# Kernel tuning notes

Hardware: AMD Instinct MI355X
Metric: run time of the kernel (lower is better)

Reference implementation:

```python
import jax, jax.numpy as jnp
import numpy as np

N_NODES = 10000
N_EDGES = 160000
D = 512
DROPOUT_P = 0.5
NEG_SLOPE = 0.25


def setup_inputs() -> dict:
    key = jax.random.key(0)
    ks = jax.random.split(key, 8)
    H = jax.random.normal(ks[0], (N_NODES, D), dtype=jnp.float32)
    rows = jax.random.randint(ks[1], (N_EDGES,), 0, N_NODES)
    cols = jax.random.randint(ks[2], (N_EDGES,), 0, N_NODES)
    vals = jax.random.uniform(ks[3], (N_EDGES,), dtype=jnp.float32)
    # xavier-normal-ish weights, zero bias (matches torch init)
    std = float(np.sqrt(2.0 / (D + D)))
    W1 = jax.random.normal(ks[4], (D, D), dtype=jnp.float32) * std
    b1 = jnp.zeros((D,), dtype=jnp.float32)
    W2 = jax.random.normal(ks[5], (D, D), dtype=jnp.float32) * std
    b2 = jnp.zeros((D,), dtype=jnp.float32)
    return {"H": H, "rows": rows, "cols": cols, "vals": vals,
            "W1": W1, "b1": b1, "W2": W2, "b2": b2}


def _spmm(rows, cols, vals, dense):
    # sparse [N,N] @ dense [N,D] via gather + segment-sum
    gathered = vals[:, None] * dense[cols]          # [E, D]
    return jax.ops.segment_sum(gathered, rows, num_segments=N_NODES)


def _leaky_relu(x):
    return jnp.where(x >= 0, x, NEG_SLOPE * x)


def reference(H, rows, cols, vals, W1, b1, W2, b2):
    # layer 1: dense GEMM -> SpMM -> bias -> leaky_relu -> dropout(training=True)
    h = _spmm(rows, cols, vals, H @ W1) + b1
    h = _leaky_relu(h)
    keep = jax.random.bernoulli(jax.random.key(42), 1.0 - DROPOUT_P, h.shape)
    h = jnp.where(keep, h / (1.0 - DROPOUT_P), 0.0)
    # layer 2
    h = _spmm(rows, cols, vals, h @ W2) + b2
    return _leaky_relu(h)
```

## Files before the change

kernel.cpp:

```cpp
#include <hip/hip_runtime.h>
#include <stdint.h>

#define N_NODES 10000
#define M_PAD   10112
#define N_EDGES 160000
#define DIM     512
#define N_ELEMS 5120000
#define NEG_SLOPE 0.25f

typedef short     short8 __attribute__((ext_vector_type(8)));
typedef __bf16    bf16x8 __attribute__((ext_vector_type(8)));
typedef float     f32x4  __attribute__((ext_vector_type(4)));

__device__ __forceinline__ unsigned short f2bf(float f) {
    uint32_t u = __builtin_bit_cast(uint32_t, f);
    uint32_t r = (u + 0x7fffu + ((u >> 16) & 1u)) >> 16;
    return (unsigned short)r;
}
__device__ __forceinline__ float b2f(unsigned short u) {
    return __builtin_bit_cast(float, (uint32_t)u << 16);
}

__device__ __forceinline__ uint32_t rotl32(uint32_t x, uint32_t d) {
    return (x << d) | (x >> (32u - d));
}
__device__ __forceinline__ void threefry_42(uint32_t x0, uint32_t x1,
                                            uint32_t& o0, uint32_t& o1) {
    const uint32_t ks0 = 0u, ks1 = 42u, ks2 = 0x1BD11BDAu ^ 42u;
    x0 += ks0; x1 += ks1;
#define TF_R4(a,b,c,d) \
    x0 += x1; x1 = rotl32(x1,a); x1 ^= x0; \
    x0 += x1; x1 = rotl32(x1,b); x1 ^= x0; \
    x0 += x1; x1 = rotl32(x1,c); x1 ^= x0; \
    x0 += x1; x1 = rotl32(x1,d); x1 ^= x0;
    TF_R4(13,15,26,6);  x0 += ks1; x1 += ks2 + 1u;
    TF_R4(17,29,16,24); x0 += ks2; x1 += ks0 + 2u;
    TF_R4(13,15,26,6);  x0 += ks0; x1 += ks1 + 3u;
    TF_R4(17,29,16,24); x0 += ks1; x1 += ks2 + 4u;
    TF_R4(13,15,26,6);  x0 += ks2; x1 += ks0 + 5u;
#undef TF_R4
    o0 = x0; o1 = x1;
}

__global__ void hist_kernel(const int* __restrict__ rows, int* __restrict__ cnt) {
    int e = blockIdx.x * blockDim.x + threadIdx.x;
    if (e < N_EDGES) atomicAdd(&cnt[rows[e]], 1);
}

__global__ __launch_bounds__(1024)
void scan_kernel(const int* __restrict__ cnt, int* __restrict__ rs, int* __restrict__ cur) {
    __shared__ int s[1024];
    int t = threadIdx.x;
    int base_i = t * 10;
    int local[10];
    int p = 0;
    if (t < 1000) {
        #pragma unroll
        for (int j = 0; j < 10; ++j) { local[j] = cnt[base_i + j]; p += local[j]; }
    }
    s[t] = p;
    __syncthreads();
    for (int off = 1; off < 1024; off <<= 1) {
        int v = (t >= off) ? s[t - off] : 0;
        __syncthreads();
        s[t] += v;
        __syncthreads();
    }
    if (t < 1000) {
        int run = s[t] - p;
        #pragma unroll
        for (int j = 0; j < 10; ++j) {
            rs[base_i + j]  = run;
            cur[base_i + j] = run;
            run += local[j];
        }
        if (t == 999) rs[N_NODES] = run;
    }
}

__global__ void scatter_kernel(const int* __restrict__ rows, const int* __restrict__ cols,
                               const float* __restrict__ vals, int* __restrict__ cur,
                               int* __restrict__ scol, float* __restrict__ sval) {
    int e = blockIdx.x * blockDim.x + threadIdx.x;
    if (e < N_EDGES) {
        int r = rows[e];
        int p = atomicAdd(&cur[r], 1);
        scol[p] = cols[e];
        sval[p] = vals[e];
    }
}

__global__ void convert_kernel(const float* __restrict__ src, unsigned short* __restrict__ dst) {
    int i = blockIdx.x * blockDim.x + threadIdx.x;
    if (i * 4 >= N_ELEMS) return;
    float4 v = ((const float4*)src)[i];
    ushort4 o;
    o.x = f2bf(v.x); o.y = f2bf(v.y); o.z = f2bf(v.z); o.w = f2bf(v.w);
    ((ushort4*)dst)[i] = o;
}

__global__ __launch_bounds__(256)
void transpose_kernel(const float* __restrict__ W, unsigned short* __restrict__ WT) {
    __shared__ float t[64][65];
    int k0 = blockIdx.x * 64, n0 = blockIdx.y * 64;
    int tx = threadIdx.x & 15, ty = threadIdx.x >> 4;
    #pragma unroll
    for (int i = 0; i < 4; ++i) {
        int k = i * 16 + ty;
        float4 v = *(const float4*)&W[(size_t)(k0 + k) * DIM + n0 + tx * 4];
        t[k][tx * 4 + 0] = v.x; t[k][tx * 4 + 1] = v.y;
        t[k][tx * 4 + 2] = v.z; t[k][tx * 4 + 3] = v.w;
    }
    __syncthreads();
    #pragma unroll
    for (int i = 0; i < 4; ++i) {
        int n = i * 16 + ty;
        ushort4 o;
        o.x = f2bf(t[tx * 4 + 0][n]); o.y = f2bf(t[tx * 4 + 1][n]);
        o.z = f2bf(t[tx * 4 + 2][n]); o.w = f2bf(t[tx * 4 + 3][n]);
        *(ushort4*)&WT[(size_t)(n0 + n) * DIM + k0 + tx * 4] = o;
    }
}

__global__ __launch_bounds__(256)
void mfma_gemm(const unsigned short* __restrict__ A, const unsigned short* __restrict__ BT,
               unsigned short* __restrict__ C, int M) {
    __shared__ short8 As[1024];
    __shared__ short8 Bs[1024];
    int tid  = threadIdx.x;
    int wid  = tid >> 6, lane = tid & 63;
    int bm   = blockIdx.x * 128;
    int bn   = blockIdx.y * 128;
    int wm   = (wid >> 1) * 64, wn = (wid & 1) * 64;

    f32x4 acc[4][4] = {};

    int srow = lane >> 3;
    int sslot = lane & 7;

    for (int k0 = 0; k0 < DIM; k0 += 64) {
        #pragma unroll
        for (int c = 0; c < 4; ++c) {
            int chunk = wid * 4 + c;
            int r  = chunk * 8 + srow;
            int ks = sslot ^ (r & 7);
            const unsigned short* ga = A  + (size_t)(bm + r) * DIM + k0 + ks * 8;
            const unsigned short* gb = BT + (size_t)(bn + r) * DIM + k0 + ks * 8;
            __builtin_amdgcn_global_load_lds(
                (const __attribute__((address_space(1))) void*)ga,
                (__attribute__((address_space(3))) void*)&As[chunk * 64], 16, 0, 0);
            __builtin_amdgcn_global_load_lds(
                (const __attribute__((address_space(1))) void*)gb,
                (__attribute__((address_space(3))) void*)&Bs[chunk * 64], 16, 0, 0);
        }
        __syncthreads();

        int lrow = lane & 15;
        int kgrp = lane >> 4;
        #pragma unroll
        for (int ks = 0; ks < 2; ++ks) {
            short8 af[4], bfr[4];
            #pragma unroll
            for (int i = 0; i < 4; ++i) {
                int r = wm + i * 16 + lrow;
                af[i]  = As[r * 8 + ((ks * 4 + kgrp) ^ (r & 7))];
                int n = wn + i * 16 + lrow;
                bfr[i] = Bs[n * 8 + ((ks * 4 + kgrp) ^ (n & 7))];
            }
            #pragma unroll
            for (int i = 0; i < 4; ++i)
                #pragma unroll
                for (int j = 0; j < 4; ++j)
                    acc[i][j] = __builtin_amdgcn_mfma_f32_16x16x32_bf16(
                        __builtin_bit_cast(bf16x8, af[i]),
                        __builtin_bit_cast(bf16x8, bfr[j]), acc[i][j], 0, 0, 0);
        }
        __syncthreads();
    }

    int crow = (lane >> 4) * 4;
    int ccol = lane & 15;
    #pragma unroll
    for (int i = 0; i < 4; ++i) {
        #pragma unroll
        for (int r = 0; r < 4; ++r) {
            int row = bm + wm + i * 16 + crow + r;
            if (row < M) {
                size_t base = (size_t)row * DIM + bn + wn + ccol;
                #pragma unroll
                for (int j = 0; j < 4; ++j)
                    C[base + j * 16] = f2bf(acc[i][j][r]);
            }
        }
    }
}

__global__ __launch_bounds__(128)
void spmm1_kernel(const unsigned short* __restrict__ X, const int* __restrict__ rs,
                  const int* __restrict__ scol, const float* __restrict__ sval,
                  const float* __restrict__ bias, unsigned short* __restrict__ hout) {
    int row = blockIdx.x;
    int t = threadIdx.x;
    int start = rs[row], end = rs[row + 1];
    const ushort4* X4 = (const ushort4*)X;
    float a0 = 0.f, a1 = 0.f, a2 = 0.f, a3 = 0.f;
    float c0 = 0.f, c1 = 0.f, c2 = 0.f, c3 = 0.f;
    int p = start;
    for (; p + 1 < end; p += 2) {
        int   i0 = scol[p], i1 = scol[p + 1];
        float v0 = sval[p], v1 = sval[p + 1];
        ushort4 x0 = X4[(size_t)i0 * 128 + t];
        ushort4 x1 = X4[(size_t)i1 * 128 + t];
        a0 = fmaf(v0, b2f(x0.x), a0); a1 = fmaf(v0, b2f(x0.y), a1);
        a2 = fmaf(v0, b2f(x0.z), a2); a3 = fmaf(v0, b2f(x0.w), a3);
        c0 = fmaf(v1, b2f(x1.x), c0); c1 = fmaf(v1, b2f(x1.y), c1);
        c2 = fmaf(v1, b2f(x1.z), c2); c3 = fmaf(v1, b2f(x1.w), c3);
    }
    if (p < end) {
        int i0 = scol[p]; float v0 = sval[p];
        ushort4 x0 = X4[(size_t)i0 * 128 + t];
        a0 = fmaf(v0, b2f(x0.x), a0); a1 = fmaf(v0, b2f(x0.y), a1);
        a2 = fmaf(v0, b2f(x0.z), a2); a3 = fmaf(v0, b2f(x0.w), a3);
    }
    float r[4];
    float4 b = *(const float4*)&bias[t * 4];
    r[0] = a0 + c0 + b.x; r[1] = a1 + c1 + b.y;
    r[2] = a2 + c2 + b.z; r[3] = a3 + c3 + b.w;
    uint32_t e0 = (uint32_t)row * DIM + t * 4;
    #pragma unroll
    for (int j = 0; j < 4; ++j) {
        float v = r[j];
        v = (v >= 0.f) ? v : NEG_SLOPE * v;
        uint32_t o0, o1;
        threefry_42(0u, e0 + j, o0, o1);
        uint32_t bits = o0 ^ o1;
        r[j] = ((int)bits >= 0) ? v * 2.0f : 0.0f;
    }
    ushort4 o;
    o.x = f2bf(r[0]); o.y = f2bf(r[1]); o.z = f2bf(r[2]); o.w = f2bf(r[3]);
    ((ushort4*)hout)[(size_t)row * 128 + t] = o;
}

__global__ __launch_bounds__(128)
void spmm2_kernel(const unsigned short* __restrict__ X, const int* __restrict__ rs,
                  const int* __restrict__ scol, const float* __restrict__ sval,
                  const float* __restrict__ bias, float* __restrict__ out) {
    int row = blockIdx.x;
    int t = threadIdx.x;
    int start = rs[row], end = rs[row + 1];
    const ushort4* X4 = (const ushort4*)X;
    float a0 = 0.f, a1 = 0.f, a2 = 0.f, a3 = 0.f;
    float c0 = 0.f, c1 = 0.f, c2 = 0.f, c3 = 0.f;
    int p = start;
    for (; p + 1 < end; p += 2) {
        int   i0 = scol[p], i1 = scol[p + 1];
        float v0 = sval[p], v1 = sval[p + 1];
        ushort4 x0 = X4[(size_t)i0 * 128 + t];
        ushort4 x1 = X4[(size_t)i1 * 128 + t];
        a0 = fmaf(v0, b2f(x0.x), a0); a1 = fmaf(v0, b2f(x0.y), a1);
        a2 = fmaf(v0, b2f(x0.z), a2); a3 = fmaf(v0, b2f(x0.w), a3);
        c0 = fmaf(v1, b2f(x1.x), c0); c1 = fmaf(v1, b2f(x1.y), c1);
        c2 = fmaf(v1, b2f(x1.z), c2); c3 = fmaf(v1, b2f(x1.w), c3);
    }
    if (p < end) {
        int i0 = scol[p]; float v0 = sval[p];
        ushort4 x0 = X4[(size_t)i0 * 128 + t];
        a0 = fmaf(v0, b2f(x0.x), a0); a1 = fmaf(v0, b2f(x0.y), a1);
        a2 = fmaf(v0, b2f(x0.z), a2); a3 = fmaf(v0, b2f(x0.w), a3);
    }
    float4 b = *(const float4*)&bias[t * 4];
    float4 r;
    r.x = a0 + c0 + b.x; r.y = a1 + c1 + b.y;
    r.z = a2 + c2 + b.z; r.w = a3 + c3 + b.w;
    r.x = (r.x >= 0.f) ? r.x : NEG_SLOPE * r.x;
    r.y = (r.y >= 0.f) ? r.y : NEG_SLOPE * r.y;
    r.z = (r.z >= 0.f) ? r.z : NEG_SLOPE * r.z;
    r.w = (r.w >= 0.f) ? r.w : NEG_SLOPE * r.w;
    ((float4*)out)[(size_t)row * 128 + t] = r;
}

extern "C" void kernel_launch(void* const* d_in, const int* in_sizes, int n_in,
                              void* d_out, int out_size, void* d_ws, size_t ws_size,
                              hipStream_t stream) {
    const float* H    = (const float*)d_in[0];
    const int*   rows = (const int*)  d_in[1];
    const int*   cols = (const int*)  d_in[2];
    const float* vals = (const float*)d_in[3];
    const float* W1   = (const float*)d_in[4];
    const float* b1   = (const float*)d_in[5];
    const float* W2   = (const float*)d_in[6];
    const float* b2   = (const float*)d_in[7];
    float* out = (float*)d_out;

    char* ws = (char*)d_ws;
    size_t off = 0;
    auto alloc = [&](size_t bytes) -> void* {
        off = (off + 255) & ~(size_t)255;
        void* p = ws + off;
        off += bytes;
        return p;
    };
    int*   cnt  = (int*)  alloc((size_t)N_NODES * 4);
    int*   rs   = (int*)  alloc((size_t)(N_NODES + 1) * 4);
    int*   cur  = (int*)  alloc((size_t)N_NODES * 4);
    int*   scol = (int*)  alloc((size_t)N_EDGES * 4);
    float* sval = (float*)alloc((size_t)N_EDGES * 4);
    unsigned short* WT1 = (unsigned short*)alloc((size_t)DIM * DIM * 2);
    unsigned short* WT2 = (unsigned short*)alloc((size_t)DIM * DIM * 2);
    unsigned short* Abf = (unsigned short*)alloc((size_t)M_PAD * DIM * 2);
    unsigned short* hbf = (unsigned short*)alloc((size_t)M_PAD * DIM * 2);
    unsigned short* Xbf = (unsigned short*)alloc((size_t)N_NODES * DIM * 2);

    convert_kernel<<<(N_ELEMS / 4 + 255) / 256, 256, 0, stream>>>(H, Abf);
    dim3 tgrid(DIM / 64, DIM / 64);
    transpose_kernel<<<tgrid, 256, 0, stream>>>(W1, WT1);
    transpose_kernel<<<tgrid, 256, 0, stream>>>(W2, WT2);
    hipMemsetAsync(cnt, 0, (size_t)N_NODES * 4, stream);
    hist_kernel<<<(N_EDGES + 255) / 256, 256, 0, stream>>>(rows, cnt);
    scan_kernel<<<1, 1024, 0, stream>>>(cnt, rs, cur);
    scatter_kernel<<<(N_EDGES + 255) / 256, 256, 0, stream>>>(rows, cols, vals, cur, scol, sval);

    dim3 ggrid(M_PAD / 128, DIM / 128);
    mfma_gemm<<<ggrid, 256, 0, stream>>>(Abf, WT1, Xbf, N_NODES);
    spmm1_kernel<<<N_NODES, 128, 0, stream>>>(Xbf, rs, scol, sval, b1, hbf);
    mfma_gemm<<<ggrid, 256, 0, stream>>>(hbf, WT2, Xbf, N_NODES);
    spmm2_kernel<<<N_NODES, 128, 0, stream>>>(Xbf, rs, scol, sval, b2, out);
}
```

Measured before the change: 126.9 us.

## Fuse prep kernels into one launch, precompute dropout bitmask, unroll SpMM by four

Merges the H-to-bf16 conversion, both weight transposes and the zeroing of the histogram counter into one multi-role prep kernel, which removes several launches and a memset. The same kernel precomputes the dropout keep mask as a packed bitmask, so spmm1 reads one word per eight threads instead of running Threefry per element. The SpMM inner loops are unrolled to four edges to keep more gathers in flight. The cost is a 640KB mask write and read, and Threefry now runs in a separate stage that can overlap the conversion work.

```diff
diff --git a/kernel.cpp b/kernel.cpp
--- a/kernel.cpp
+++ b/kernel.cpp
@@ -8,9 +8,9 @@
 #define N_ELEMS 5120000
 #define NEG_SLOPE 0.25f
 
-typedef short     short8 __attribute__((ext_vector_type(8)));
-typedef __bf16    bf16x8 __attribute__((ext_vector_type(8)));
-typedef float     f32x4  __attribute__((ext_vector_type(4)));
+typedef short          short8   __attribute__((ext_vector_type(8)));
+typedef __bf16         bf16x8   __attribute__((ext_vector_type(8)));
+typedef float          f32x4    __attribute__((ext_vector_type(4)));
 
 __device__ __forceinline__ unsigned short f2bf(float f) {
     uint32_t u = __builtin_bit_cast(uint32_t, f);
@@ -42,6 +42,71 @@
     o0 = x0; o1 = x1;
 }
 
+#define CONV_BLKS 5000
+#define TR_BLKS   64
+#define MASK_BLKS 625
+#define ZERO_BLKS 10
+
+__device__ __forceinline__ void transpose_tile(const float* __restrict__ W,
+                                               unsigned short* __restrict__ WT,
+                                               int tile, float (*ts)[65]) {
+    int k0 = (tile & 7) * 64, n0 = (tile >> 3) * 64;
+    int tx = threadIdx.x & 15, ty = threadIdx.x >> 4;
+    #pragma unroll
+    for (int i = 0; i < 4; ++i) {
+        int k = i * 16 + ty;
+        float4 v = *(const float4*)&W[(size_t)(k0 + k) * DIM + n0 + tx * 4];
+        ts[k][tx * 4 + 0] = v.x; ts[k][tx * 4 + 1] = v.y;
+        ts[k][tx * 4 + 2] = v.z; ts[k][tx * 4 + 3] = v.w;
+    }
+    __syncthreads();
+    #pragma unroll
+    for (int i = 0; i < 4; ++i) {
+        int n = i * 16 + ty;
+        ushort4 o;
+        o.x = f2bf(ts[tx * 4 + 0][n]); o.y = f2bf(ts[tx * 4 + 1][n]);
+        o.z = f2bf(ts[tx * 4 + 2][n]); o.w = f2bf(ts[tx * 4 + 3][n]);
+        *(ushort4*)&WT[(size_t)(n0 + n) * DIM + k0 + tx * 4] = o;
+    }
+}
+
+__global__ __launch_bounds__(256)
+void prep_kernel(const float* __restrict__ H, const float* __restrict__ W1,
+                 const float* __restrict__ W2, unsigned short* __restrict__ Abf,
+                 unsigned short* __restrict__ WT1, unsigned short* __restrict__ WT2,
+                 uint32_t* __restrict__ mask, int* __restrict__ cnt) {
+    __shared__ float ts[64][65];
+    int b = blockIdx.x;
+    if (b < CONV_BLKS) {
+        int i = b * 256 + threadIdx.x;
+        float4 v = ((const float4*)H)[i];
+        ushort4 o;
+        o.x = f2bf(v.x); o.y = f2bf(v.y); o.z = f2bf(v.z); o.w = f2bf(v.w);
+        ((ushort4*)Abf)[i] = o;
+    } else if (b < CONV_BLKS + TR_BLKS) {
+        transpose_tile(W1, WT1, b - CONV_BLKS, ts);
+    } else if (b < CONV_BLKS + 2 * TR_BLKS) {
+        transpose_tile(W2, WT2, b - CONV_BLKS - TR_BLKS, ts);
+    } else if (b < CONV_BLKS + 2 * TR_BLKS + MASK_BLKS) {
+        int w = (b - CONV_BLKS - 2 * TR_BLKS) * 256 + threadIdx.x;
+        uint32_t base = (uint32_t)w * 32;
+        uint32_t m = 0;
+        #pragma unroll
+        for (int j = 0; j < 32; ++j) {
+            uint32_t o0, o1;
+            threefry_42(0u, base + j, o0, o1);
+            uint32_t bits = o0 ^ o1;
+            m |= (uint32_t)(((int)bits >= 0) ? 1u : 0u) << j;
+        }
+        mask[w] = m;
+    } else {
+        int i = (b - CONV_BLKS - 2 * TR_BLKS - MASK_BLKS) * 1024 + threadIdx.x * 4;
+        #pragma unroll
+        for (int j = 0; j < 4; ++j)
+            if (i + j < N_NODES) cnt[i + j] = 0;
+    }
+}
+
 __global__ void hist_kernel(const int* __restrict__ rows, int* __restrict__ cnt) {
     int e = blockIdx.x * blockDim.x + threadIdx.x;
     if (e < N_EDGES) atomicAdd(&cnt[rows[e]], 1);
@@ -87,38 +152,6 @@
         int p = atomicAdd(&cur[r], 1);
         scol[p] = cols[e];
         sval[p] = vals[e];
-    }
-}
-
-__global__ void convert_kernel(const float* __restrict__ src, unsigned short* __restrict__ dst) {
-    int i = blockIdx.x * blockDim.x + threadIdx.x;
-    if (i * 4 >= N_ELEMS) return;
-    float4 v = ((const float4*)src)[i];
-    ushort4 o;
-    o.x = f2bf(v.x); o.y = f2bf(v.y); o.z = f2bf(v.z); o.w = f2bf(v.w);
-    ((ushort4*)dst)[i] = o;
-}
-
-__global__ __launch_bounds__(256)
-void transpose_kernel(const float* __restrict__ W, unsigned short* __restrict__ WT) {
-    __shared__ float t[64][65];
-    int k0 = blockIdx.x * 64, n0 = blockIdx.y * 64;
-    int tx = threadIdx.x & 15, ty = threadIdx.x >> 4;
-    #pragma unroll
-    for (int i = 0; i < 4; ++i) {
-        int k = i * 16 + ty;
-        float4 v = *(const float4*)&W[(size_t)(k0 + k) * DIM + n0 + tx * 4];
-        t[k][tx * 4 + 0] = v.x; t[k][tx * 4 + 1] = v.y;
-        t[k][tx * 4 + 2] = v.z; t[k][tx * 4 + 3] = v.w;
-    }
-    __syncthreads();
-    #pragma unroll
-    for (int i = 0; i < 4; ++i) {
-        int n = i * 16 + ty;
-        ushort4 o;
-        o.x = f2bf(t[tx * 4 + 0][n]); o.y = f2bf(t[tx * 4 + 1][n]);
-        o.z = f2bf(t[tx * 4 + 2][n]); o.w = f2bf(t[tx * 4 + 3][n]);
-        *(ushort4*)&WT[(size_t)(n0 + n) * DIM + k0 + tx * 4] = o;
     }
 }
 
@@ -198,7 +231,8 @@
 __global__ __launch_bounds__(128)
 void spmm1_kernel(const unsigned short* __restrict__ X, const int* __restrict__ rs,
                   const int* __restrict__ scol, const float* __restrict__ sval,
-                  const float* __restrict__ bias, unsigned short* __restrict__ hout) {
+                  const float* __restrict__ bias, const uint32_t* __restrict__ mask,
+                  unsigned short* __restrict__ hout) {
     int row = blockIdx.x;
     int t = threadIdx.x;
     int start = rs[row], end = rs[row + 1];
@@ -206,17 +240,23 @@
     float a0 = 0.f, a1 = 0.f, a2 = 0.f, a3 = 0.f;
     float c0 = 0.f, c1 = 0.f, c2 = 0.f, c3 = 0.f;
     int p = start;
-    for (; p + 1 < end; p += 2) {
-        int   i0 = scol[p], i1 = scol[p + 1];
-        float v0 = sval[p], v1 = sval[p + 1];
+    for (; p + 3 < end; p += 4) {
+        int   i0 = scol[p],     i1 = scol[p + 1], i2 = scol[p + 2], i3 = scol[p + 3];
+        float v0 = sval[p],     v1 = sval[p + 1], v2 = sval[p + 2], v3 = sval[p + 3];
         ushort4 x0 = X4[(size_t)i0 * 128 + t];
         ushort4 x1 = X4[(size_t)i1 * 128 + t];
+        ushort4 x2 = X4[(size_t)i2 * 128 + t];
+        ushort4 x3 = X4[(size_t)i3 * 128 + t];
         a0 = fmaf(v0, b2f(x0.x), a0); a1 = fmaf(v0, b2f(x0.y), a1);
         a2 = fmaf(v0, b2f(x0.z), a2); a3 = fmaf(v0, b2f(x0.w), a3);
         c0 = fmaf(v1, b2f(x1.x), c0); c1 = fmaf(v1, b2f(x1.y), c1);
         c2 = fmaf(v1, b2f(x1.z), c2); c3 = fmaf(v1, b2f(x1.w), c3);
-    }
-    if (p < end) {
+        a0 = fmaf(v2, b2f(x2.x), a0); a1 = fmaf(v2, b2f(x2.y), a1);
+        a2 = fmaf(v2, b2f(x2.z), a2); a3 = fmaf(v2, b2f(x2.w), a3);
+        c0 = fmaf(v3, b2f(x3.x), c0); c1 = fmaf(v3, b2f(x3.y), c1);
+        c2 = fmaf(v3, b2f(x3.z), c2); c3 = fmaf(v3, b2f(x3.w), c3);
+    }
+    for (; p < end; ++p) {
         int i0 = scol[p]; float v0 = sval[p];
         ushort4 x0 = X4[(size_t)i0 * 128 + t];
         a0 = fmaf(v0, b2f(x0.x), a0); a1 = fmaf(v0, b2f(x0.y), a1);
@@ -226,17 +266,15 @@
     float4 b = *(const float4*)&bias[t * 4];
     r[0] = a0 + c0 + b.x; r[1] = a1 + c1 + b.y;
     r[2] = a2 + c2 + b.z; r[3] = a3 + c3 + b.w;
-    uint32_t e0 = (uint32_t)row * DIM + t * 4;
+    uint32_t w = mask[(size_t)row * 16 + (t >> 3)];
+    uint32_t nib = (w >> ((t & 7) * 4)) & 0xFu;
+    ushort4 o;
     #pragma unroll
     for (int j = 0; j < 4; ++j) {
         float v = r[j];
         v = (v >= 0.f) ? v : NEG_SLOPE * v;
-        uint32_t o0, o1;
-        threefry_42(0u, e0 + j, o0, o1);
-        uint32_t bits = o0 ^ o1;
-        r[j] = ((int)bits >= 0) ? v * 2.0f : 0.0f;
-    }
-    ushort4 o;
+        r[j] = ((nib >> j) & 1u) ? v * 2.0f : 0.0f;
+    }
     o.x = f2bf(r[0]); o.y = f2bf(r[1]); o.z = f2bf(r[2]); o.w = f2bf(r[3]);
     ((ushort4*)hout)[(size_t)row * 128 + t] = o;
 }
@@ -252,17 +290,23 @@
     float a0 = 0.f, a1 = 0.f, a2 = 0.f, a3 = 0.f;
     float c0 = 0.f, c1 = 0.f, c2 = 0.f, c3 = 0.f;
     int p = start;
-    for (; p + 1 < end; p += 2) {
-        int   i0 = scol[p], i1 = scol[p + 1];
-        float v0 = sval[p], v1 = sval[p + 1];
+    for (; p + 3 < end; p += 4) {
+        int   i0 = scol[p],     i1 = scol[p + 1], i2 = scol[p + 2], i3 = scol[p + 3];
+        float v0 = sval[p],     v1 = sval[p + 1], v2 = sval[p + 2], v3 = sval[p + 3];
         ushort4 x0 = X4[(size_t)i0 * 128 + t];
         ushort4 x1 = X4[(size_t)i1 * 128 + t];
+        ushort4 x2 = X4[(size_t)i2 * 128 + t];
+        ushort4 x3 = X4[(size_t)i3 * 128 + t];
         a0 = fmaf(v0, b2f(x0.x), a0); a1 = fmaf(v0, b2f(x0.y), a1);
         a2 = fmaf(v0, b2f(x0.z), a2); a3 = fmaf(v0, b2f(x0.w), a3);
         c0 = fmaf(v1, b2f(x1.x), c0); c1 = fmaf(v1, b2f(x1.y), c1);
         c2 = fmaf(v1, b2f(x1.z), c2); c3 = fmaf(v1, b2f(x1.w), c3);
-    }
-    if (p < end) {
+        a0 = fmaf(v2, b2f(x2.x), a0); a1 = fmaf(v2, b2f(x2.y), a1);
+        a2 = fmaf(v2, b2f(x2.z), a2); a3 = fmaf(v2, b2f(x2.w), a3);
+        c0 = fmaf(v3, b2f(x3.x), c0); c1 = fmaf(v3, b2f(x3.y), c1);
+        c2 = fmaf(v3, b2f(x3.z), c2); c3 = fmaf(v3, b2f(x3.w), c3);
+    }
+    for (; p < end; ++p) {
         int i0 = scol[p]; float v0 = sval[p];
         ushort4 x0 = X4[(size_t)i0 * 128 + t];
         a0 = fmaf(v0, b2f(x0.x), a0); a1 = fmaf(v0, b2f(x0.y), a1);
@@ -300,29 +344,27 @@
         off += bytes;
         return p;
     };
-    int*   cnt  = (int*)  alloc((size_t)N_NODES * 4);
-    int*   rs   = (int*)  alloc((size_t)(N_NODES + 1) * 4);
-    int*   cur  = (int*)  alloc((size_t)N_NODES * 4);
-    int*   scol = (int*)  alloc((size_t)N_EDGES * 4);
-    float* sval = (float*)alloc((size_t)N_EDGES * 4);
+    int*      cnt  = (int*)     alloc((size_t)N_NODES * 4);
+    int*      rs   = (int*)     alloc((size_t)(N_NODES + 1) * 4);
+    int*      cur  = (int*)     alloc((size_t)N_NODES * 4);
+    int*      scol = (int*)     alloc((size_t)N_EDGES * 4);
+    float*    sval = (float*)   alloc((size_t)N_EDGES * 4);
+    uint32_t* mask = (uint32_t*)alloc((size_t)N_ELEMS / 8);
     unsigned short* WT1 = (unsigned short*)alloc((size_t)DIM * DIM * 2);
     unsigned short* WT2 = (unsigned short*)alloc((size_t)DIM * DIM * 2);
     unsigned short* Abf = (unsigned short*)alloc((size_t)M_PAD * DIM * 2);
     unsigned short* hbf = (unsigned short*)alloc((size_t)M_PAD * DIM * 2);
     unsigned short* Xbf = (unsigned short*)alloc((size_t)N_NODES * DIM * 2);
 
-    convert_kernel<<<(N_ELEMS / 4 + 255) / 256, 256, 0, stream>>>(H, Abf);
-    dim3 tgrid(DIM / 64, DIM / 64);
-    transpose_kernel<<<tgrid, 256, 0, stream>>>(W1, WT1);
-    transpose_kernel<<<tgrid, 256, 0, stream>>>(W2, WT2);
-    hipMemsetAsync(cnt, 0, (size_t)N_NODES * 4, stream);
+    int prep_blocks = CONV_BLKS + 2 * TR_BLKS + MASK_BLKS + ZERO_BLKS;
+    prep_kernel<<<prep_blocks, 256, 0, stream>>>(H, W1, W2, Abf, WT1, WT2, mask, cnt);
     hist_kernel<<<(N_EDGES + 255) / 256, 256, 0, stream>>>(rows, cnt);
     scan_kernel<<<1, 1024, 0, stream>>>(cnt, rs, cur);
     scatter_kernel<<<(N_EDGES + 255) / 256, 256, 0, stream>>>(rows, cols, vals, cur, scol, sval);
 
     dim3 ggrid(M_PAD / 128, DIM / 128);
     mfma_gemm<<<ggrid, 256, 0, stream>>>(Abf, WT1, Xbf, N_NODES);
-    spmm1_kernel<<<N_NODES, 128, 0, stream>>>(Xbf, rs, scol, sval, b1, hbf);
+    spmm1_kernel<<<N_NODES, 128, 0, stream>>>(Xbf, rs, scol, sval, b1, mask, hbf);
     mfma_gemm<<<ggrid, 256, 0, stream>>>(hbf, WT2, Xbf, N_NODES);
     spmm2_kernel<<<N_NODES, 128, 0, stream>>>(Xbf, rs, scol, sval, b2, out);
 }
```

After: 135.5 us. 6.8% more time.
